# Kernel tuning notes

Hardware: AMD Instinct MI355X
Metric: run time of the kernel (lower is better)

Reference implementation:

```python
import jax, jax.numpy as jnp
import numpy as np

D_MODEL = 768
D_STATE = 16
EXPAND = 2
D_INNER = D_MODEL * EXPAND
K_CONV = 4
RMS_EPS = 1.1920928955078125e-07  # torch.finfo(float32).eps (nn.RMSNorm default eps=None)


def setup_inputs() -> dict:
    key = jax.random.key(0)
    ks = jax.random.split(key, 8)
    x = jax.random.normal(ks[0], (2, 2048, D_MODEL), dtype=jnp.float32)
    # parameters (torch Linear stores [out, in]; we keep that layout and use x @ W.T)
    in_proj_w = jax.random.normal(ks[1], (2 * D_INNER, D_MODEL), jnp.float32) * (1.0 / np.sqrt(D_MODEL))
    conv_w = jax.random.normal(ks[2], (D_INNER, 1, K_CONV), jnp.float32) * (1.0 / np.sqrt(K_CONV))
    conv_b = jax.random.normal(ks[3], (D_INNER,), jnp.float32) * 0.1
    x_proj_w = jax.random.normal(ks[4], (2 * D_STATE, D_INNER), jnp.float32) * (1.0 / np.sqrt(D_INNER))
    dt_proj_w = jax.random.normal(ks[5], (D_INNER, D_INNER), jnp.float32) * (1.0 / np.sqrt(D_INNER))
    dt_proj_b = jax.random.normal(ks[6], (D_INNER,), jnp.float32) * 0.1
    A_log = jnp.log(jnp.broadcast_to(jnp.arange(1, D_STATE + 1, dtype=jnp.float32)[None, :], (D_INNER, D_STATE)))
    D_skip = jnp.ones((D_INNER,), jnp.float32)
    out_proj_w = jax.random.normal(ks[7], (D_MODEL, D_INNER), jnp.float32) * (1.0 / np.sqrt(D_INNER))
    norm_w = jnp.ones((D_MODEL,), jnp.float32)
    return {"x": x, "norm_w": norm_w, "in_proj_w": in_proj_w, "conv_w": conv_w,
            "conv_b": conv_b, "x_proj_w": x_proj_w, "dt_proj_w": dt_proj_w,
            "dt_proj_b": dt_proj_b, "A_log": A_log, "D_skip": D_skip,
            "out_proj_w": out_proj_w}


def reference(x, norm_w, in_proj_w, conv_w, conv_b, x_proj_w, dt_proj_w,
              dt_proj_b, A_log, D_skip, out_proj_w):
    # x: [B, L, d_model]
    residual = x
    xn = x * jax.lax.rsqrt(jnp.mean(x * x, axis=-1, keepdims=True) + RMS_EPS) * norm_w
    xz = xn @ in_proj_w.T                       # [B, L, 2*d_inner]
    d_inner = in_proj_w.shape[0] // 2
    xb, z = xz[..., :d_inner], xz[..., d_inner:]
    # causal depthwise conv: torch pads 3 both sides then truncates to L == left-pad 3
    xc = jax.lax.conv_general_dilated(
        xb.transpose(0, 2, 1), conv_w, window_strides=(1,), padding=[(K_CONV - 1, 0)],
        feature_group_count=d_inner, dimension_numbers=("NCH", "OIH", "NCH"))
    xc = xc + conv_b[None, :, None]
    u = jax.nn.silu(xc.transpose(0, 2, 1))      # [B, L, d_inner]
    bc = u @ x_proj_w.T                          # [B, L, 2*d_state]
    N = A_log.shape[1]
    Bp, Cp = bc[..., :N], bc[..., N:]
    delta = jax.nn.softplus(u @ dt_proj_w.T + dt_proj_b)  # [B, L, d_inner]
    A = -jnp.exp(A_log)                          # [d_inner, N]

    def step(h, ins):
        dl, ut, Bt, Ct = ins                     # [B,D], [B,D], [B,N], [B,N]
        dA = jnp.exp(dl[:, :, None] * A)         # [B, D, N]
        h = dA * h + dl[:, :, None] * Bt[:, None, :] * ut[:, :, None]
        y = jnp.einsum("bdn,bn->bd", h, Ct)
        return h, y

    B_, L, _ = u.shape
    h0 = jnp.zeros((B_, d_inner, N), x.dtype)
    xs = (delta.transpose(1, 0, 2), u.transpose(1, 0, 2),
          Bp.transpose(1, 0, 2), Cp.transpose(1, 0, 2))
    _, ys = jax.lax.scan(step, h0, xs)           # ys: [L, B, d_inner]
    y = ys.transpose(1, 0, 2) + u * D_skip
    out = (y * jax.nn.silu(z)) @ out_proj_w.T
    return out + residual
```

## Files before the change

### kernel.cpp

```cpp
#include <hip/hip_runtime.h>
#include <math.h>

#define DM 768
#define DI 1536
#define NS 16
#define LL 2048
#define MROWS 4096
#define CH 32
#define NC 64

using bf16x8 = __attribute__((ext_vector_type(8))) short;
using f32x4 = __attribute__((ext_vector_type(4))) float;

__device__ __forceinline__ float4 ld4(const float* p) { return *(const float4*)p; }

__device__ __forceinline__ unsigned short f2bf(float f) {
  unsigned int u = __float_as_uint(f);
  u += 0x7fff + ((u >> 16) & 1);
  return (unsigned short)(u >> 16);
}
__device__ __forceinline__ float b2f(unsigned short s) {
  return __uint_as_float(((unsigned int)s) << 16);
}

__device__ __forceinline__ void gload16(const void* g, void* l) {
  __builtin_amdgcn_global_load_lds((const __attribute__((address_space(1))) void*)g,
                                   (__attribute__((address_space(3))) void*)l, 16, 0, 0);
}

#define N4_IN 589824
#define N4_CAT 638976
#define N4_OUT 294912
__global__ __launch_bounds__(256) void cvt_all(const float* __restrict__ ipw,
                                               const float* __restrict__ dtw,
                                               const float* __restrict__ xpw,
                                               const float* __restrict__ opw,
                                               unsigned short* __restrict__ d_in4,
                                               unsigned short* __restrict__ d_cat,
                                               unsigned short* __restrict__ d_out4) {
  int i = blockIdx.x * 256 + threadIdx.x;
  if (i < N4_IN) {
    float4 v = ld4(ipw + (size_t)i * 4);
    ushort4 o = {f2bf(v.x), f2bf(v.y), f2bf(v.z), f2bf(v.w)};
    *(ushort4*)(d_in4 + (size_t)i * 4) = o;
  } else if (i < N4_IN + N4_CAT) {
    int j = i - N4_IN;
    int row = j / 384;
    int col = (j % 384) * 4;
    ushort4 o = {0, 0, 0, 0};
    if (row < 1536) {
      float4 v = ld4(dtw + (size_t)row * DI + col);
      o = {f2bf(v.x), f2bf(v.y), f2bf(v.z), f2bf(v.w)};
    } else if (row < 1568) {
      float4 v = ld4(xpw + (size_t)(row - 1536) * DI + col);
      o = {f2bf(v.x), f2bf(v.y), f2bf(v.z), f2bf(v.w)};
    }
    *(ushort4*)(d_cat + (size_t)j * 4) = o;
  } else if (i < N4_IN + N4_CAT + N4_OUT) {
    int j = i - N4_IN - N4_CAT;
    float4 v = ld4(opw + (size_t)j * 4);
    ushort4 o = {f2bf(v.x), f2bf(v.y), f2bf(v.z), f2bf(v.w)};
    *(ushort4*)(d_out4 + (size_t)j * 4) = o;
  }
}

__global__ __launch_bounds__(256) void rmsnorm_kernel(const float* __restrict__ x,
                                                      const float* __restrict__ w,
                                                      unsigned short* __restrict__ xn) {
  int row = blockIdx.x;
  const float* xr = x + (size_t)row * DM;
  unsigned short* xo = xn + (size_t)row * DM;
  int tid = threadIdx.x;
  float v0 = xr[tid], v1 = xr[tid + 256], v2 = xr[tid + 512];
  float ss = v0 * v0 + v1 * v1 + v2 * v2;
#pragma unroll
  for (int o = 32; o > 0; o >>= 1) ss += __shfl_xor(ss, o, 64);
  __shared__ float red[4];
  if ((tid & 63) == 0) red[tid >> 6] = ss;
  __syncthreads();
  float tot = red[0] + red[1] + red[2] + red[3];
  float sc = rsqrtf(tot * (1.0f / 768.0f) + 1.1920928955078125e-07f);
  xo[tid] = f2bf(v0 * sc * w[tid]);
  xo[tid + 256] = f2bf(v1 * sc * w[tid + 256]);
  xo[tid + 512] = f2bf(v2 * sc * w[tid + 512]);
}

template <int EPI, int BM, int BN>
__global__ __launch_bounds__(256) void mfma_gemm(const unsigned short* __restrict__ A,
                                                 const unsigned short* __restrict__ Bw,
                                                 const float* __restrict__ bias,
                                                 const float* __restrict__ resid,
                                                 void* __restrict__ o0v,
                                                 void* __restrict__ o1v, int K, int gx) {
  constexpr int NFI = BM / 32;
  constexpr int NFJ = BN / 32;
  constexpr int NCH = (BM + BN) / 8;
  __shared__ unsigned short As[2][BM * 64];
  __shared__ unsigned short Bs[2][BN * 64];
  int tid = threadIdx.x;
  int lane = tid & 63, w = tid >> 6;
  int wr = w >> 1, wc = w & 1;

  int nwg = gx * gridDim.y;
  int orig = blockIdx.y * gx + blockIdx.x;
  int q = nwg >> 3;
  int swz = (orig & 7) * q + (orig >> 3);
  int bm = (swz / gx) * BM, bn = (swz % gx) * BN;

  f32x4 acc[NFI][NFJ];
#pragma unroll
  for (int i = 0; i < NFI; i++)
#pragma unroll
    for (int j = 0; j < NFJ; j++) acc[i][j] = (f32x4){0.f, 0.f, 0.f, 0.f};

  const unsigned short* Ab = A + (size_t)bm * K;
  const unsigned short* Bb = Bw + (size_t)bn * K;
  int lrow = lane >> 3;
  int kof = ((lane & 7) ^ lrow) * 8;

  auto stage = [&](int buf, int k0) {
#pragma unroll
    for (int ch = w; ch < NCH; ch += 4) {
      if (ch < BM / 8) {
        int row = ch * 8 + lrow;
        gload16(Ab + (size_t)row * K + k0 + kof, &As[buf][ch * 512]);
      } else {
        int row = (ch - BM / 8) * 8 + lrow;
        gload16(Bb + (size_t)row * K + k0 + kof, &Bs[buf][(ch - BM / 8) * 512]);
      }
    }
  };
  auto compute = [&](int buf) {
#pragma unroll
    for (int kk = 0; kk < 2; kk++) {
      int sa = (((kk * 4) + (lane >> 4)) ^ (lane & 7)) * 8;
      bf16x8 af[NFI], bfr[NFJ];
#pragma unroll
      for (int i = 0; i < NFI; i++) {
        int arow = wr * (BM / 2) + i * 16 + (lane & 15);
        af[i] = *(const bf16x8*)&As[buf][arow * 64 + sa];
      }
#pragma unroll
      for (int j = 0; j < NFJ; j++) {
        int brow = wc * (BN / 2) + j * 16 + (lane & 15);
        bfr[j] = *(const bf16x8*)&Bs[buf][brow * 64 + sa];
      }
#pragma unroll
      for (int i = 0; i < NFI; i++)
#pragma unroll
        for (int j = 0; j < NFJ; j++)
          acc[i][j] = __builtin_amdgcn_mfma_f32_16x16x32_bf16(af[i], bfr[j], acc[i][j], 0, 0, 0);
    }
  };

  int nk = K >> 6;
  stage(0, 0);
  for (int t = 0; t < nk; t++) {
    if (t + 1 < nk) {
      stage((t + 1) & 1, (t + 1) << 6);
      asm volatile("s_waitcnt vmcnt(4)" ::: "memory");
    } else {
      asm volatile("s_waitcnt vmcnt(0)" ::: "memory");
    }
    __builtin_amdgcn_s_barrier();
    compute(t & 1);
    __builtin_amdgcn_s_barrier();
  }

#pragma unroll
  for (int i = 0; i < NFI; i++) {
#pragma unroll
    for (int j = 0; j < NFJ; j++) {
      int row0 = bm + wr * (BM / 2) + i * 16 + (lane >> 4) * 4;
      int col = bn + wc * (BN / 2) + j * 16 + (lane & 15);
#pragma unroll
      for (int r = 0; r < 4; r++) {
        float v = acc[i][j][r];
        int row = row0 + r;
        if (EPI == 0) {
          unsigned short* xb = (unsigned short*)o0v;
          unsigned short* z = (unsigned short*)o1v;
          if (col < DI) xb[(size_t)row * DI + col] = f2bf(v);
          else z[(size_t)row * DI + col - DI] = f2bf(v);
        } else if (EPI == 1) {
          float* delta = (float*)o0v;
          float* bc = (float*)o1v;
          if (col < DI) {
            v += bias[col];
            v = (v > 20.0f) ? v : log1pf(expf(v));
            delta[(size_t)row * DI + col] = v;
          } else if (col < DI + 2 * NS) {
            bc[(size_t)row * 32 + col - DI] = v;
          }
        } else {
          float* out = (float*)o0v;
          out[(size_t)row * DM + col] = v + resid[(size_t)row * DM + col];
        }
      }
    }
  }
}

__global__ __launch_bounds__(192) void conv_silu_kernel(const unsigned short* __restrict__ xb,
                                                        const float* __restrict__ cw,
                                                        const float* __restrict__ cb,
                                                        unsigned short* __restrict__ u) {
  int d = (blockIdx.x * 192 + threadIdx.x) << 2;
  int m = blockIdx.y;
  int t = m & (LL - 1);
  float4 w0 = ld4(cw + d * 4);
  float4 w1 = ld4(cw + d * 4 + 4);
  float4 w2 = ld4(cw + d * 4 + 8);
  float4 w3 = ld4(cw + d * 4 + 12);
  float4 acc = {cb[d], cb[d + 1], cb[d + 2], cb[d + 3]};
#pragma unroll
  for (int tap = 0; tap < 4; tap++) {
    int dt_ = 3 - tap;
    if (t >= dt_) {
      ushort4 xv = *(const ushort4*)(xb + (size_t)(m - dt_) * DI + d);
      float wx = (tap == 0) ? w0.x : (tap == 1) ? w0.y : (tap == 2) ? w0.z : w0.w;
      float wy = (tap == 0) ? w1.x : (tap == 1) ? w1.y : (tap == 2) ? w1.z : w1.w;
      float wz = (tap == 0) ? w2.x : (tap == 1) ? w2.y : (tap == 2) ? w2.z : w2.w;
      float ww = (tap == 0) ? w3.x : (tap == 1) ? w3.y : (tap == 2) ? w3.z : w3.w;
      acc.x += b2f(xv.x) * wx;
      acc.y += b2f(xv.y) * wy;
      acc.z += b2f(xv.z) * wz;
      acc.w += b2f(xv.w) * ww;
    }
  }
  ushort4 o = {f2bf(acc.x / (1.0f + __expf(-acc.x))), f2bf(acc.y / (1.0f + __expf(-acc.y))),
               f2bf(acc.z / (1.0f + __expf(-acc.z))), f2bf(acc.w / (1.0f + __expf(-acc.w)))};
  *(ushort4*)(u + (size_t)m * DI + d) = o;
}

__global__ __launch_bounds__(256) void scan_pass1(const float* __restrict__ delta,
                                                  const unsigned short* __restrict__ u,
                                                  const float* __restrict__ bc,
                                                  const float* __restrict__ A_log,
                                                  float* __restrict__ chunkP,
                                                  float* __restrict__ chunkS) {
  int d = blockIdx.x * 256 + threadIdx.x;
  int c = blockIdx.y;
  int b = blockIdx.z;
  float Acoef[NS];
#pragma unroll
  for (int n = 0; n < NS; n++) Acoef[n] = -__expf(A_log[d * NS + n]);
  __shared__ float sB[CH][NS];
  const float* bcb = bc + (size_t)(b * LL + c * CH) * 32;
  for (int i = threadIdx.x; i < CH * NS; i += 256) sB[i >> 4][i & 15] = bcb[(i >> 4) * 32 + (i & 15)];
  __syncthreads();
  float P[NS], S[NS];
#pragma unroll
  for (int n = 0; n < NS; n++) { P[n] = 1.f; S[n] = 0.f; }
  int m0 = b * LL + c * CH;
  for (int tt = 0; tt < CH; tt++) {
    size_t off = (size_t)(m0 + tt) * DI + d;
    float dl = delta[off];
    float ut = b2f(u[off]);
    float dlu = dl * ut;
#pragma unroll
    for (int n = 0; n < NS; n++) {
      float dA = __expf(dl * Acoef[n]);
      S[n] = dA * S[n] + dlu * sB[tt][n];
      P[n] *= dA;
    }
  }
  size_t base = ((size_t)(b * NC + c) * NS) * DI + d;
#pragma unroll
  for (int n = 0; n < NS; n++) {
    chunkP[base + (size_t)n * DI] = P[n];
    chunkS[base + (size_t)n * DI] = S[n];
  }
}

__global__ __launch_bounds__(256) void scan_pass2(const float* __restrict__ chunkP,
                                                  float* __restrict__ chunkS) {
  int id = blockIdx.x * 256 + threadIdx.x;
  int d = id % DI;
  int n = (id / DI) % NS;
  int b = id / (DI * NS);
  float h = 0.f;
  for (int c = 0; c < NC; c++) {
    size_t idx = ((size_t)(b * NC + c) * NS + n) * DI + d;
    float p = chunkP[idx];
    float s = chunkS[idx];
    chunkS[idx] = h;
    h = p * h + s;
  }
}

__global__ __launch_bounds__(256) void scan_pass3(const float* __restrict__ delta,
                                                  const unsigned short* __restrict__ u,
                                                  const float* __restrict__ bc,
                                                  const float* __restrict__ hIn,
                                                  const float* __restrict__ A_log,
                                                  const float* __restrict__ D_skip,
                                                  const unsigned short* __restrict__ z,
                                                  unsigned short* __restrict__ yg) {
  int d = blockIdx.x * 256 + threadIdx.x;
  int c = blockIdx.y;
  int b = blockIdx.z;
  float Acoef[NS];
#pragma unroll
  for (int n = 0; n < NS; n++) Acoef[n] = -__expf(A_log[d * NS + n]);
  float Dsk = D_skip[d];
  __shared__ float sBC[CH][32];
  const float* bcb = bc + (size_t)(b * LL + c * CH) * 32;
  for (int i = threadIdx.x; i < CH * 32; i += 256) sBC[i >> 5][i & 31] = bcb[i];
  __syncthreads();
  float h[NS];
  size_t base = ((size_t)(b * NC + c) * NS) * DI + d;
#pragma unroll
  for (int n = 0; n < NS; n++) h[n] = hIn[base + (size_t)n * DI];
  int m0 = b * LL + c * CH;
  for (int tt = 0; tt < CH; tt++) {
    size_t m = (size_t)(m0 + tt);
    size_t off = m * DI + d;
    float dl = delta[off];
    float ut = b2f(u[off]);
    float dlu = dl * ut;
    float yt = 0.f;
#pragma unroll
    for (int n = 0; n < NS; n++) {
      float dA = __expf(dl * Acoef[n]);
      h[n] = dA * h[n] + dlu * sBC[tt][n];
      yt += h[n] * sBC[tt][16 + n];
    }
    float zv = b2f(z[m * DI + d]);
    float sz = zv / (1.0f + __expf(-zv));
    yg[m * DI + d] = f2bf((yt + ut * Dsk) * sz);
  }
}

extern "C" void kernel_launch(void* const* d_in, const int* in_sizes, int n_in,
                              void* d_out, int out_size, void* d_ws, size_t ws_size,
                              hipStream_t stream) {
  const float* x = (const float*)d_in[0];
  const float* norm_w = (const float*)d_in[1];
  const float* in_proj_w = (const float*)d_in[2];
  const float* conv_w = (const float*)d_in[3];
  const float* conv_b = (const float*)d_in[4];
  const float* x_proj_w = (const float*)d_in[5];
  const float* dt_proj_w = (const float*)d_in[6];
  const float* dt_proj_b = (const float*)d_in[7];
  const float* A_log = (const float*)d_in[8];
  const float* D_skip = (const float*)d_in[9];
  const float* out_proj_w = (const float*)d_in[10];
  float* out = (float*)d_out;

  float* ws = (float*)d_ws;
  unsigned short* xb_bf = (unsigned short*)ws;
  unsigned short* z_bf = (unsigned short*)(ws + 3145728);
  unsigned short* u_bf = (unsigned short*)(ws + 6291456);
  float* delta = ws + 9437184;
  unsigned short* ygbf = (unsigned short*)(ws + 15728640);
  unsigned short* wbf_in = (unsigned short*)(ws + 18874368);
  unsigned short* wbf_cat = (unsigned short*)(ws + 20054016);
  unsigned short* wbf_out = (unsigned short*)(ws + 21331968);
  float* chunkP = ws + 21921792;
  float* chunkS = ws + 25067520;
  unsigned short* xn_bf = (unsigned short*)d_out;
  float* bcb = (float*)d_out + 1572864;

  cvt_all<<<5953, 256, 0, stream>>>(in_proj_w, dt_proj_w, x_proj_w, out_proj_w,
                                    wbf_in, wbf_cat, wbf_out);

  rmsnorm_kernel<<<4096, 256, 0, stream>>>(x, norm_w, xn_bf);

  mfma_gemm<0, 64, 64><<<dim3(48, 64), 256, 0, stream>>>(xn_bf, wbf_in, nullptr, nullptr,
                                                         xb_bf, z_bf, DM, 48);

  conv_silu_kernel<<<dim3(2, 4096), 192, 0, stream>>>(xb_bf, conv_w, conv_b, u_bf);

  mfma_gemm<1, 64, 64><<<dim3(26, 64), 256, 0, stream>>>(u_bf, wbf_cat, dt_proj_b, nullptr,
                                                         delta, bcb, DI, 26);

  scan_pass1<<<dim3(6, NC, 2), 256, 0, stream>>>(delta, u_bf, bcb, A_log, chunkP, chunkS);
  scan_pass2<<<192, 256, 0, stream>>>(chunkP, chunkS);
  scan_pass3<<<dim3(6, NC, 2), 256, 0, stream>>>(delta, u_bf, bcb, chunkS, A_log, D_skip,
                                                 z_bf, ygbf);

  mfma_gemm<2, 64, 64><<<dim3(12, 64), 256, 0, stream>>>(ygbf, wbf_out, nullptr, x, out,
                                                         nullptr, DI, 12);
}
```

Before: 223.6 us.

## Store delta in bf16, triple-buffer GEMM loads, merge rmsnorm into weight-convert kernel

The softplus delta tensor is now written as bf16 instead of fp32, which halves its write traffic in the dt GEMM and its read traffic in both scan passes. The GEMM moves from double to triple-buffered LDS staging with two tiles in flight and a barrier at the top of each iteration. The RMSNorm kernel is folded into the weight-conversion kernel as extra blocks to save one launch. Risks are lower delta precision in the scan and higher LDS use per block, which could reduce occupancy.

```diff
diff --git a/kernel.cpp b/kernel.cpp
--- a/kernel.cpp
+++ b/kernel.cpp
@@ -31,14 +31,38 @@
 #define N4_IN 589824
 #define N4_CAT 638976
 #define N4_OUT 294912
-__global__ __launch_bounds__(256) void cvt_all(const float* __restrict__ ipw,
-                                               const float* __restrict__ dtw,
-                                               const float* __restrict__ xpw,
-                                               const float* __restrict__ opw,
-                                               unsigned short* __restrict__ d_in4,
-                                               unsigned short* __restrict__ d_cat,
-                                               unsigned short* __restrict__ d_out4) {
-  int i = blockIdx.x * 256 + threadIdx.x;
+#define CVT_BLOCKS 5953
+__global__ __launch_bounds__(256) void prep_kernel(const float* __restrict__ ipw,
+                                                   const float* __restrict__ dtw,
+                                                   const float* __restrict__ xpw,
+                                                   const float* __restrict__ opw,
+                                                   unsigned short* __restrict__ d_in4,
+                                                   unsigned short* __restrict__ d_cat,
+                                                   unsigned short* __restrict__ d_out4,
+                                                   const float* __restrict__ x,
+                                                   const float* __restrict__ nw,
+                                                   unsigned short* __restrict__ xn) {
+  int blk = blockIdx.x;
+  int tid = threadIdx.x;
+  if (blk >= CVT_BLOCKS) {
+    int row = blk - CVT_BLOCKS;
+    const float* xr = x + (size_t)row * DM;
+    unsigned short* xo = xn + (size_t)row * DM;
+    float v0 = xr[tid], v1 = xr[tid + 256], v2 = xr[tid + 512];
+    float ss = v0 * v0 + v1 * v1 + v2 * v2;
+#pragma unroll
+    for (int o = 32; o > 0; o >>= 1) ss += __shfl_xor(ss, o, 64);
+    __shared__ float red[4];
+    if ((tid & 63) == 0) red[tid >> 6] = ss;
+    __syncthreads();
+    float tot = red[0] + red[1] + red[2] + red[3];
+    float sc = rsqrtf(tot * (1.0f / 768.0f) + 1.1920928955078125e-07f);
+    xo[tid] = f2bf(v0 * sc * nw[tid]);
+    xo[tid + 256] = f2bf(v1 * sc * nw[tid + 256]);
+    xo[tid + 512] = f2bf(v2 * sc * nw[tid + 512]);
+    return;
+  }
+  int i = blk * 256 + tid;
   if (i < N4_IN) {
     float4 v = ld4(ipw + (size_t)i * 4);
     ushort4 o = {f2bf(v.x), f2bf(v.y), f2bf(v.z), f2bf(v.w)};
@@ -64,27 +88,6 @@
   }
 }
 
-__global__ __launch_bounds__(256) void rmsnorm_kernel(const float* __restrict__ x,
-                                                      const float* __restrict__ w,
-                                                      unsigned short* __restrict__ xn) {
-  int row = blockIdx.x;
-  const float* xr = x + (size_t)row * DM;
-  unsigned short* xo = xn + (size_t)row * DM;
-  int tid = threadIdx.x;
-  float v0 = xr[tid], v1 = xr[tid + 256], v2 = xr[tid + 512];
-  float ss = v0 * v0 + v1 * v1 + v2 * v2;
-#pragma unroll
-  for (int o = 32; o > 0; o >>= 1) ss += __shfl_xor(ss, o, 64);
-  __shared__ float red[4];
-  if ((tid & 63) == 0) red[tid >> 6] = ss;
-  __syncthreads();
-  float tot = red[0] + red[1] + red[2] + red[3];
-  float sc = rsqrtf(tot * (1.0f / 768.0f) + 1.1920928955078125e-07f);
-  xo[tid] = f2bf(v0 * sc * w[tid]);
-  xo[tid + 256] = f2bf(v1 * sc * w[tid + 256]);
-  xo[tid + 512] = f2bf(v2 * sc * w[tid + 512]);
-}
-
 template <int EPI, int BM, int BN>
 __global__ __launch_bounds__(256) void mfma_gemm(const unsigned short* __restrict__ A,
                                                  const unsigned short* __restrict__ Bw,
@@ -95,8 +98,8 @@
   constexpr int NFI = BM / 32;
   constexpr int NFJ = BN / 32;
   constexpr int NCH = (BM + BN) / 8;
-  __shared__ unsigned short As[2][BM * 64];
-  __shared__ unsigned short Bs[2][BN * 64];
+  __shared__ unsigned short As[3][BM * 64];
+  __shared__ unsigned short Bs[3][BN * 64];
   int tid = threadIdx.x;
   int lane = tid & 63, w = tid >> 6;
   int wr = w >> 1, wc = w & 1;
@@ -155,16 +158,22 @@
 
   int nk = K >> 6;
   stage(0, 0);
+  stage(1, 64);
+  int buf = 0;
   for (int t = 0; t < nk; t++) {
-    if (t + 1 < nk) {
-      stage((t + 1) & 1, (t + 1) << 6);
+    __builtin_amdgcn_s_barrier();
+    if (t + 2 < nk) {
+      int b2 = buf + 2; if (b2 >= 3) b2 -= 3;
+      stage(b2, (t + 2) << 6);
+      asm volatile("s_waitcnt vmcnt(8)" ::: "memory");
+    } else if (t + 1 < nk) {
       asm volatile("s_waitcnt vmcnt(4)" ::: "memory");
     } else {
       asm volatile("s_waitcnt vmcnt(0)" ::: "memory");
     }
     __builtin_amdgcn_s_barrier();
-    compute(t & 1);
-    __builtin_amdgcn_s_barrier();
+    compute(buf);
+    buf = (buf == 2) ? 0 : buf + 1;
   }
 
 #pragma unroll
@@ -183,12 +192,12 @@
           if (col < DI) xb[(size_t)row * DI + col] = f2bf(v);
           else z[(size_t)row * DI + col - DI] = f2bf(v);
         } else if (EPI == 1) {
-          float* delta = (float*)o0v;
+          unsigned short* delta = (unsigned short*)o0v;
           float* bc = (float*)o1v;
           if (col < DI) {
             v += bias[col];
             v = (v > 20.0f) ? v : log1pf(expf(v));
-            delta[(size_t)row * DI + col] = v;
+            delta[(size_t)row * DI + col] = f2bf(v);
           } else if (col < DI + 2 * NS) {
             bc[(size_t)row * 32 + col - DI] = v;
           }
@@ -233,7 +242,7 @@
   *(ushort4*)(u + (size_t)m * DI + d) = o;
 }
 
-__global__ __launch_bounds__(256) void scan_pass1(const float* __restrict__ delta,
+__global__ __launch_bounds__(256) void scan_pass1(const unsigned short* __restrict__ delta,
                                                   const unsigned short* __restrict__ u,
                                                   const float* __restrict__ bc,
                                                   const float* __restrict__ A_log,
@@ -255,7 +264,7 @@
   int m0 = b * LL + c * CH;
   for (int tt = 0; tt < CH; tt++) {
     size_t off = (size_t)(m0 + tt) * DI + d;
-    float dl = delta[off];
+    float dl = b2f(delta[off]);
     float ut = b2f(u[off]);
     float dlu = dl * ut;
 #pragma unroll
@@ -289,7 +298,7 @@
   }
 }
 
-__global__ __launch_bounds__(256) void scan_pass3(const float* __restrict__ delta,
+__global__ __launch_bounds__(256) void scan_pass3(const unsigned short* __restrict__ delta,
                                                   const unsigned short* __restrict__ u,
                                                   const float* __restrict__ bc,
                                                   const float* __restrict__ hIn,
@@ -316,7 +325,7 @@
   for (int tt = 0; tt < CH; tt++) {
     size_t m = (size_t)(m0 + tt);
     size_t off = m * DI + d;
-    float dl = delta[off];
+    float dl = b2f(delta[off]);
     float ut = b2f(u[off]);
     float dlu = dl * ut;
     float yt = 0.f;
@@ -352,7 +361,7 @@
   unsigned short* xb_bf = (unsigned short*)ws;
   unsigned short* z_bf = (unsigned short*)(ws + 3145728);
   unsigned short* u_bf = (unsigned short*)(ws + 6291456);
-  float* delta = ws + 9437184;
+  unsigned short* delta_bf = (unsigned short*)(ws + 9437184);
   unsigned short* ygbf = (unsigned short*)(ws + 15728640);
   unsigned short* wbf_in = (unsigned short*)(ws + 18874368);
   unsigned short* wbf_cat = (unsigned short*)(ws + 20054016);
@@ -362,10 +371,9 @@
   unsigned short* xn_bf = (unsigned short*)d_out;
   float* bcb = (float*)d_out + 1572864;
 
-  cvt_all<<<5953, 256, 0, stream>>>(in_proj_w, dt_proj_w, x_proj_w, out_proj_w,
-                                    wbf_in, wbf_cat, wbf_out);
-
-  rmsnorm_kernel<<<4096, 256, 0, stream>>>(x, norm_w, xn_bf);
+  prep_kernel<<<CVT_BLOCKS + 4096, 256, 0, stream>>>(in_proj_w, dt_proj_w, x_proj_w,
+                                                     out_proj_w, wbf_in, wbf_cat, wbf_out,
+                                                     x, norm_w, xn_bf);
 
   mfma_gemm<0, 64, 64><<<dim3(48, 64), 256, 0, stream>>>(xn_bf, wbf_in, nullptr, nullptr,
                                                          xb_bf, z_bf, DM, 48);
@@ -373,11 +381,11 @@
   conv_silu_kernel<<<dim3(2, 4096), 192, 0, stream>>>(xb_bf, conv_w, conv_b, u_bf);
 
   mfma_gemm<1, 64, 64><<<dim3(26, 64), 256, 0, stream>>>(u_bf, wbf_cat, dt_proj_b, nullptr,
-                                                         delta, bcb, DI, 26);
-
-  scan_pass1<<<dim3(6, NC, 2), 256, 0, stream>>>(delta, u_bf, bcb, A_log, chunkP, chunkS);
+                                                         delta_bf, bcb, DI, 26);
+
+  scan_pass1<<<dim3(6, NC, 2), 256, 0, stream>>>(delta_bf, u_bf, bcb, A_log, chunkP, chunkS);
   scan_pass2<<<192, 256, 0, stream>>>(chunkP, chunkS);
-  scan_pass3<<<dim3(6, NC, 2), 256, 0, stream>>>(delta, u_bf, bcb, chunkS, A_log, D_skip,
+  scan_pass3<<<dim3(6, NC, 2), 256, 0, stream>>>(delta_bf, u_bf, bcb, chunkS, A_log, D_skip,
                                                  z_bf, ygbf);
 
   mfma_gemm<2, 64, 64><<<dim3(12, 64), 256, 0, stream>>>(ygbf, wbf_out, nullptr, x, out,
```

Measured after the change: 220.5 us. About the same (-1.4%).
